# Optimization experiments

Hardware: AMD Instinct MI355X
Metric: run time of the kernel (lower is better)

## Reference

```python
import jax, jax.numpy as jnp
import numpy as np

N_NODES = 50000
N_EDGES = 800000
D_IN = 128
D_OUT = 128


def setup_inputs() -> dict:
    key = jax.random.key(0)
    k1, k2, k3, k4, k5 = jax.random.split(key, 5)
    x = jax.random.normal(k1, (N_NODES, D_IN), dtype=jnp.float32)
    edge_index = jax.random.randint(k2, (2, N_EDGES), 0, N_NODES, dtype=jnp.int64)
    # PyG SAGEConv params: lin_l (neighbors, with bias), lin_r (root, no bias)
    scale = 1.0 / np.sqrt(D_IN)
    W_l = jax.random.uniform(k3, (D_OUT, D_IN), dtype=jnp.float32, minval=-scale, maxval=scale)
    b_l = jax.random.uniform(k4, (D_OUT,), dtype=jnp.float32, minval=-scale, maxval=scale)
    W_r = jax.random.uniform(k5, (D_OUT, D_IN), dtype=jnp.float32, minval=-scale, maxval=scale)
    return {"x": x, "edge_index": edge_index, "W_l": W_l, "b_l": b_l, "W_r": W_r}


def reference(x, edge_index, W_l, b_l, W_r):
    src, dst = edge_index[0], edge_index[1]
    # mean aggregation of neighbor (source) features into destination nodes
    msg = x[src]  # [E, D_IN]
    agg_sum = jax.ops.segment_sum(msg, dst, num_segments=N_NODES)  # [N, D_IN]
    deg = jax.ops.segment_sum(jnp.ones((N_EDGES,), dtype=x.dtype), dst, num_segments=N_NODES)
    agg = agg_sum / jnp.maximum(deg, 1.0)[:, None]  # isolated nodes -> 0
    # out = lin_l(agg) + lin_r(x); ReLU from SAGE_NET wrapper (active=True)
    out = agg @ W_l.T + b_l + x @ W_r.T
    return jax.nn.relu(out)
```

## Files before the change

kernel.cpp:

```cpp
#include <hip/hip_runtime.h>
#include <hip/hip_bf16.h>

#define NNODES 50000
#define NEDGES 800000
#define DD 128
#define NPART 8
#define PSIZE 6250
#define CAP 64
#define NGROUPS 3910
#define WK_B (NGROUPS * 8 + 64)
#define WP2 68
#define ZROW ((u32)NNODES)

typedef unsigned int u32;
typedef unsigned short u16;
typedef short bf16x8 __attribute__((ext_vector_type(8)));
typedef float f32x4 __attribute__((ext_vector_type(4)));
typedef float f32x2 __attribute__((ext_vector_type(2)));

#if defined(__has_builtin)
#if __has_builtin(__builtin_amdgcn_cvt_pk_f32_fp8)
#define HAVE_HW_FP8 1
#endif
#endif

union U4B8 {
    uint4 u;
    bf16x8 b;
};

__device__ __forceinline__ u32 f2b(float f) {
    u32 u = __float_as_uint(f);
    u32 rounding = 0x7fffu + ((u >> 16) & 1u);
    return (u + rounding) >> 16;
}

__device__ __forceinline__ u32 f2e4m3(float f) {
    u32 u = __float_as_uint(f);
    u32 s = (u >> 31) << 7;
    u32 mag = u & 0x7fffffffu;
    if (mag < 0x3c800000u) return s;
    u32 t = mag + 0x0007FFFFu + ((mag >> 20) & 1u);
    u32 e = (t >> 23) - 120u;
    u32 m = (t >> 20) & 7u;
    if (e > 15u || (e == 15u && m == 7u)) { e = 15u; m = 6u; }
    return s | (e << 3) | m;
}

__device__ __forceinline__ void fp8x4_acc(u32 v, float& a0, float& a1,
                                          float& a2, float& a3) {
#ifdef HAVE_HW_FP8
    f32x2 lo = __builtin_amdgcn_cvt_pk_f32_fp8((int)v, false);
    f32x2 hi = __builtin_amdgcn_cvt_pk_f32_fp8((int)v, true);
    a0 += lo.x;
    a1 += lo.y;
    a2 += hi.x;
    a3 += hi.y;
#else
#pragma unroll
    for (int b = 0; b < 4; ++b) {
        u32 byte = (v >> (8 * b)) & 0xffu;
        u32 f = ((byte >> 7) << 31) | ((((byte >> 3) & 15u) + 120u) << 23) |
                ((byte & 7u) << 20);
        float val = (byte & 0x78u) ? __uint_as_float(f) : 0.f;
        if (b == 0) a0 += val;
        else if (b == 1) a1 += val;
        else if (b == 2) a2 += val;
        else a3 += val;
    }
#endif
}

__global__ __launch_bounds__(256) void work_k(
    const int* __restrict__ ei, u32* __restrict__ deg,
    u16* __restrict__ slots16, const float* __restrict__ x,
    u32* __restrict__ xb, u32* __restrict__ xq,
    const float* __restrict__ Wl, const float* __restrict__ Wr,
    u32* __restrict__ wb) {
    const int b = blockIdx.x, tid = threadIdx.x;
    if (b < NGROUPS * 8) {
        const u32 g = (u32)b >> 3, r8 = (u32)b & 7u;
        const u32 gm = g % 5u, gq = g / 5u;
        if (gm < 4u) {
            u32 fg = gq * 4u + gm;
            if (fg < 3125u) {
                u32 e = fg * 256u + tid;
                int dst = ei[NEDGES + e];
                if ((u32)(dst - r8 * PSIZE) < (u32)PSIZE) {
                    u32 pos = atomicAdd(deg + dst, 1u);
                    if (pos < CAP) slots16[(size_t)dst * CAP + pos] = (u16)ei[e];
                }
            }
        } else {
            u32 xi = gq * 8u + r8;
            if (xi < 6250u) {
                int i = (int)xi * 256 + tid;
                float4 v = ((const float4*)x)[i];
                uint2 o;
                o.x = f2b(v.x) | (f2b(v.y) << 16);
                o.y = f2b(v.z) | (f2b(v.w) << 16);
                ((uint2*)xb)[i] = o;
                xq[i] = f2e4m3(v.x) | (f2e4m3(v.y) << 8) | (f2e4m3(v.z) << 16) |
                        (f2e4m3(v.w) << 24);
            }
        }
    } else {
        int idx = (b - NGROUPS * 8) * 256 + tid;
        int o = idx >> 7, c = idx & 127, k0 = 2 * c;
        const float* src = (k0 < DD) ? (Wl + o * DD + k0) : (Wr + o * DD + (k0 - DD));
        wb[idx] = f2b(src[0]) | (f2b(src[1]) << 16);
        if (b == WK_B - 1 && tid < 32)
            xq[(size_t)ZROW * 32 + tid] = 0u;
    }
}

__global__ __launch_bounds__(512, 4) void sage_fused_k(
    const u32* __restrict__ xq, const u16* __restrict__ slots16,
    const u32* __restrict__ deg, const u32* __restrict__ xb,
    const u32* __restrict__ wb, const float* __restrict__ bl,
    float* __restrict__ out) {
    __shared__ u32 w2[DD * WP2];
    __shared__ u32 agg_lds[64 * WP2];
    __shared__ float sbias[DD];
    const int tid = threadIdx.x;
    const int row0 = blockIdx.x * 64;
    const int wave = tid >> 6, lane = tid & 63;
    const int m = lane & 15, quad = lane >> 4;
    const int rw = wave & 3;
    const int ch = wave >> 2;

    for (int r = tid >> 5; r < DD; r += 16) {
        int c2 = (tid & 31) * 2;
        *(uint2*)&w2[r * WP2 + c2] = *(const uint2*)&wb[r * DD + c2];
    }
    if (tid < DD) sbias[tid] = bl[tid];

    uint4 af_x[4];
    {
        int r = row0 + rw * 16 + m;
        r = r < NNODES ? r : NNODES - 1;
        const u32* xrow = xb + (size_t)r * 64;
#pragma unroll
        for (int ks = 0; ks < 4; ++ks)
            af_x[ks] = *(const uint4*)&xrow[ks * 16 + quad * 4];
    }

    const u32 half = lane >> 5;
    const u32 q = lane & 31u;
    const u32 nbase = (u32)(row0 + wave * 8);

    u32 dv[8], svv[8];
#pragma unroll
    for (int i = 0; i < 8; ++i) {
        u32 nn = nbase + (u32)i;
        bool ok = nn < (u32)NNODES;
        dv[i] = ok ? deg[nn] : 0u;
        svv[i] = ok ? (u32)slots16[(size_t)nn * CAP + lane] : 0u;
    }

#pragma unroll
    for (int i = 0; i < 8; ++i) {
        u32 d = dv[i];
        u32 cnt = min(d, (u32)CAP);
        u32 svp = (lane < cnt) ? svv[i] : ZROW;
        float a0 = 0.f, a1 = 0.f, a2 = 0.f, a3 = 0.f;
        for (u32 j = 0; j < cnt; j += 16) {
            u32 v[8];
#pragma unroll
            for (int p = 0; p < 8; ++p) {
                u32 sA = __shfl(svp, (int)(j + 2 * p), 64);
                u32 sB = __shfl(svp, (int)(j + 2 * p + 1), 64);
                u32 s = half ? sB : sA;
                v[p] = xq[(size_t)s * 32 + q];
            }
#pragma unroll
            for (int p = 0; p < 8; ++p) fp8x4_acc(v[p], a0, a1, a2, a3);
        }
        a0 += __shfl_xor(a0, 32, 64);
        a1 += __shfl_xor(a1, 32, 64);
        a2 += __shfl_xor(a2, 32, 64);
        a3 += __shfl_xor(a3, 32, 64);
        if (lane < 32) {
            float inv = 1.0f / fmaxf((float)d, 1.0f);
            uint2 o;
            o.x = f2b(a0 * inv) | (f2b(a1 * inv) << 16);
            o.y = f2b(a2 * inv) | (f2b(a3 * inv) << 16);
            *(uint2*)&agg_lds[(wave * 8 + i) * WP2 + q * 2] = o;
        }
    }
    __syncthreads();

    f32x4 acc[4];
#pragma unroll
    for (int nt = 0; nt < 4; ++nt) acc[nt] = (f32x4){0.f, 0.f, 0.f, 0.f};

#pragma unroll
    for (int ks = 0; ks < 4; ++ks) {
        U4B8 af;
        af.u = *(const uint4*)&agg_lds[(rw * 16 + m) * WP2 + ks * 16 + quad * 4];
#pragma unroll
        for (int nt = 0; nt < 4; ++nt) {
            U4B8 bf;
            bf.u = *(const uint4*)&w2[((ch * 4 + nt) * 16 + m) * WP2 + ks * 16 +
                                      quad * 4];
            acc[nt] = __builtin_amdgcn_mfma_f32_16x16x32_bf16(af.b, bf.b,
                                                              acc[nt], 0, 0, 0);
        }
    }
    __syncthreads();
    for (int r = tid >> 5; r < DD; r += 16) {
        int c2 = (tid & 31) * 2;
        *(uint2*)&w2[r * WP2 + c2] = *(const uint2*)&wb[r * DD + 64 + c2];
    }
    __syncthreads();

#pragma unroll
    for (int ks = 0; ks < 4; ++ks) {
        U4B8 af;
        af.u = af_x[ks];
#pragma unroll
        for (int nt = 0; nt < 4; ++nt) {
            U4B8 bf;
            bf.u = *(const uint4*)&w2[((ch * 4 + nt) * 16 + m) * WP2 + ks * 16 +
                                      quad * 4];
            acc[nt] = __builtin_amdgcn_mfma_f32_16x16x32_bf16(af.b, bf.b,
                                                              acc[nt], 0, 0, 0);
        }
    }

#pragma unroll
    for (int nt = 0; nt < 4; ++nt) {
        int col = (ch * 4 + nt) * 16 + m;
        float b = sbias[col];
#pragma unroll
        for (int r_ = 0; r_ < 4; ++r_) {
            int row = row0 + rw * 16 + quad * 4 + r_;
            if (row < NNODES)
                out[(size_t)row * DD + col] = fmaxf(acc[nt][r_] + b, 0.f);
        }
    }
}

__global__ __launch_bounds__(256) void scatter_k(
    const float* __restrict__ x, const int* __restrict__ ei,
    float* __restrict__ agg, u32* __restrict__ deg) {
    u32 gid = blockIdx.x * 256u + threadIdx.x;
    u32 edge = gid >> 6;
    u32 lane = gid & 63u;
    if (edge >= NEDGES) return;
    int src = ei[edge];
    int dst = ei[NEDGES + edge];
    float2 v = ((const float2*)(x + (size_t)src * DD))[lane];
    float* p = agg + (size_t)dst * DD + lane * 2u;
    unsafeAtomicAdd(p, v.x);
    unsafeAtomicAdd(p + 1, v.y);
    if (lane == 0) atomicAdd(deg + dst, 1u);
}

__global__ __launch_bounds__(256) void mean_k(
    float* __restrict__ agg, const u32* __restrict__ deg) {
    u32 gid = blockIdx.x * 256u + threadIdx.x;
    u32 node = gid >> 6;
    u32 lane = gid & 63u;
    if (node >= NNODES) return;
    float inv = 1.0f / fmaxf((float)deg[node], 1.0f);
    float2* p = (float2*)(agg + (size_t)node * DD) + lane;
    float2 v = *p;
    *p = make_float2(v.x * inv, v.y * inv);
}

__global__ __launch_bounds__(256) void lin_l_k(
    float* __restrict__ agg,
    const float* __restrict__ Wl, const float* __restrict__ bl) {
    __shared__ u32 WT[DD * 65];
    __shared__ float rows[4 * DD];
    __shared__ float sbias[DD];
    const int tid = threadIdx.x;
    {
        u16* WTs = (u16*)WT;
        for (int i = tid; i < DD * DD; i += 256) {
            int o = i >> 7, k = i & 127;
            WTs[k * 130 + o] = (u16)f2b(Wl[i]);
        }
        if (tid < DD) sbias[tid] = bl[tid];
    }
    __syncthreads();
    const int h = tid & 63;
    const int nl = tid >> 6;
    for (int base = blockIdx.x * 4; base < NNODES; base += gridDim.x * 4) {
        ((float2*)rows)[tid] =
            ((const float2*)(agg + (size_t)(base + (tid >> 6)) * DD))[tid & 63];
        __syncthreads();
        float acc0 = sbias[2 * h], acc1 = sbias[2 * h + 1];
#pragma unroll
        for (int k = 0; k < DD; ++k) {
            float a = rows[nl * DD + k];
            u32 w2 = WT[k * 65 + h];
            acc0 = fmaf(a, __uint_as_float(w2 << 16), acc0);
            acc1 = fmaf(a, __uint_as_float(w2 & 0xffff0000u), acc1);
        }
        __syncthreads();
        ((float2*)(agg + (size_t)(base + nl) * DD))[h] = make_float2(acc0, acc1);
    }
}

__global__ __launch_bounds__(256) void lin_r_k(
    float* __restrict__ io, const float* __restrict__ x,
    const float* __restrict__ Wr) {
    __shared__ u32 WT[DD * 65];
    __shared__ float rows[4 * DD];
    const int tid = threadIdx.x;
    {
        u16* WTs = (u16*)WT;
        for (int i = tid; i < DD * DD; i += 256) {
            int o = i >> 7, k = i & 127;
            WTs[k * 130 + o] = (u16)f2b(Wr[i]);
        }
    }
    __syncthreads();
    const int h = tid & 63;
    const int nl = tid >> 6;
    for (int base = blockIdx.x * 4; base < NNODES; base += gridDim.x * 4) {
        ((float2*)rows)[tid] =
            ((const float2*)(x + (size_t)(base + (tid >> 6)) * DD))[tid & 63];
        __syncthreads();
        float2 t2 = ((const float2*)(io + (size_t)(base + nl) * DD))[h];
        float acc0 = t2.x, acc1 = t2.y;
#pragma unroll
        for (int k = 0; k < DD; ++k) {
            float a = rows[nl * DD + k];
            u32 w2 = WT[k * 65 + h];
            acc0 = fmaf(a, __uint_as_float(w2 << 16), acc0);
            acc1 = fmaf(a, __uint_as_float(w2 & 0xffff0000u), acc1);
        }
        acc0 = fmaxf(acc0, 0.f);
        acc1 = fmaxf(acc1, 0.f);
        __syncthreads();
        ((float2*)(io + (size_t)(base + nl) * DD))[h] = make_float2(acc0, acc1);
    }
}

extern "C" void kernel_launch(void* const* d_in, const int* in_sizes, int n_in,
                              void* d_out, int out_size, void* d_ws, size_t ws_size,
                              hipStream_t stream) {
    const float* x  = (const float*)d_in[0];
    const int*   ei = (const int*)d_in[1];
    const float* Wl = (const float*)d_in[2];
    const float* bl = (const float*)d_in[3];
    const float* Wr = (const float*)d_in[4];

    u32* deg     = (u32*)d_ws;
    u16* slots16 = (u16*)(deg + NNODES);
    u32* wb      = (u32*)d_ws + NNODES + (size_t)NNODES * (CAP / 2);
    u32* xb      = wb + 16384;
    u32* xq      = xb + (size_t)NNODES * 64;
    const size_t need =
        ((size_t)NNODES * (1 + CAP / 2 + 64 + 32) + 16384 + 32) * 4;

    if (ws_size >= need) {
        hipMemsetAsync(deg, 0, (size_t)NNODES * sizeof(u32), stream);
        work_k<<<WK_B, 256, 0, stream>>>(
            ei, deg, slots16, x, xb, xq, Wl, Wr, wb);
        sage_fused_k<<<(NNODES + 63) / 64, 512, 0, stream>>>(
            xq, slots16, deg, xb, wb, bl, (float*)d_out);
    } else {
        float* agg = (float*)d_out;
        hipMemsetAsync(d_out, 0, (size_t)NNODES * DD * sizeof(float), stream);
        hipMemsetAsync(d_ws, 0, (size_t)NNODES * sizeof(u32), stream);
        scatter_k<<<(NEDGES * 64) / 256, 256, 0, stream>>>(x, ei, agg, deg);
        mean_k<<<(NNODES * 64 + 255) / 256, 256, 0, stream>>>(agg, deg);
        lin_l_k<<<1024, 256, 0, stream>>>(agg, Wl, bl);
        lin_r_k<<<1024, 256, 0, stream>>>(agg, x, Wr);
    }
}
```

Baseline: 163.7 us.

## Software-pipeline neighbor gathers across batches and nodes in aggregation loop

Restructures the per-wave mean-aggregation loop into a flat software pipeline: the next batch of 16 fp8 neighbor-row loads is issued (including the first batch of the next node) before the current batch is accumulated, hiding gather latency across node boundaries. The up-front loading of all 8 nodes' degree and slot lists is replaced by a one-node-ahead prefetch, and the x-row fragment loads for the MFMA are moved after the aggregation phase. This doubles the gather register buffers and adds loop-control branching, which may raise VGPR pressure and reduce occupancy.

```diff
diff --git a/kernel.cpp b/kernel.cpp
--- a/kernel.cpp
+++ b/kernel.cpp
@@ -69,6 +69,17 @@
         else a3 += val;
     }
 #endif
+}
+
+__device__ __forceinline__ void issue8(const u32* __restrict__ xq, u32 svp,
+                                       u32 j, u32 half, u32 q, u32 v[8]) {
+#pragma unroll
+    for (int p = 0; p < 8; ++p) {
+        u32 sA = __shfl(svp, (int)(j + 2u * p), 64);
+        u32 sB = __shfl(svp, (int)(j + 2u * p + 1u), 64);
+        u32 s = half ? sB : sA;
+        v[p] = xq[(size_t)s * 32 + q];
+    }
 }
 
 __global__ __launch_bounds__(256) void work_k(
@@ -135,6 +146,80 @@
     }
     if (tid < DD) sbias[tid] = bl[tid];
 
+    const u32 half = lane >> 5;
+    const u32 q = lane & 31u;
+    const u32 nbase = (u32)(row0 + wave * 8);
+
+    u32 d_cur = 0, sv_cur = 0;
+    if (nbase < (u32)NNODES) {
+        d_cur = deg[nbase];
+        sv_cur = (u32)slots16[(size_t)nbase * CAP + lane];
+    }
+    u32 d_nxt = 0, sv_nxt = 0;
+    if (nbase + 1u < (u32)NNODES) {
+        d_nxt = deg[nbase + 1u];
+        sv_nxt = (u32)slots16[(size_t)(nbase + 1u) * CAP + lane];
+    }
+
+    u32 cnt = min(d_cur, (u32)CAP);
+    u32 nb = cnt ? ((cnt + 15u) >> 4) : 1u;
+    u32 svp = (lane < cnt) ? sv_cur : ZROW;
+    u32 ddiv = d_cur;
+
+    float a0 = 0.f, a1 = 0.f, a2 = 0.f, a3 = 0.f;
+    u32 vb[8], vn[8];
+    issue8(xq, svp, 0u, half, q, vb);
+
+    int i = 0;
+    u32 b = 0;
+    u32 cnt_n = 0, nb_n = 0, svp_n = 0, ddiv_n = 0;
+    for (;;) {
+        const bool last_b = (b + 1u >= nb);
+        const bool have_next = !(last_b && i == 7);
+        if (have_next) {
+            if (!last_b) {
+                issue8(xq, svp, (b + 1u) * 16u, half, q, vn);
+            } else {
+                cnt_n = min(d_nxt, (u32)CAP);
+                nb_n = cnt_n ? ((cnt_n + 15u) >> 4) : 1u;
+                svp_n = (lane < cnt_n) ? sv_nxt : ZROW;
+                ddiv_n = d_nxt;
+                issue8(xq, svp_n, 0u, half, q, vn);
+            }
+        }
+#pragma unroll
+        for (int p = 0; p < 8; ++p) fp8x4_acc(vb[p], a0, a1, a2, a3);
+        if (last_b) {
+            a0 += __shfl_xor(a0, 32, 64);
+            a1 += __shfl_xor(a1, 32, 64);
+            a2 += __shfl_xor(a2, 32, 64);
+            a3 += __shfl_xor(a3, 32, 64);
+            if (lane < 32) {
+                float inv = 1.0f / fmaxf((float)ddiv, 1.0f);
+                uint2 o;
+                o.x = f2b(a0 * inv) | (f2b(a1 * inv) << 16);
+                o.y = f2b(a2 * inv) | (f2b(a3 * inv) << 16);
+                *(uint2*)&agg_lds[(wave * 8 + i) * WP2 + q * 2] = o;
+            }
+            a0 = a1 = a2 = a3 = 0.f;
+            ++i;
+            if (i == 8) break;
+            cnt = cnt_n; nb = nb_n; svp = svp_n; ddiv = ddiv_n;
+            b = 0;
+            u32 nn = nbase + (u32)i + 1u;
+            d_nxt = 0; sv_nxt = 0;
+            if (i < 7 && nn < (u32)NNODES) {
+                d_nxt = deg[nn];
+                sv_nxt = (u32)slots16[(size_t)nn * CAP + lane];
+            }
+        } else {
+            ++b;
+        }
+#pragma unroll
+        for (int p = 0; p < 8; ++p) vb[p] = vn[p];
+    }
+    __syncthreads();
+
     uint4 af_x[4];
     {
         int r = row0 + rw * 16 + m;
@@ -144,51 +229,6 @@
         for (int ks = 0; ks < 4; ++ks)
             af_x[ks] = *(const uint4*)&xrow[ks * 16 + quad * 4];
     }
-
-    const u32 half = lane >> 5;
-    const u32 q = lane & 31u;
-    const u32 nbase = (u32)(row0 + wave * 8);
-
-    u32 dv[8], svv[8];
-#pragma unroll
-    for (int i = 0; i < 8; ++i) {
-        u32 nn = nbase + (u32)i;
-        bool ok = nn < (u32)NNODES;
-        dv[i] = ok ? deg[nn] : 0u;
-        svv[i] = ok ? (u32)slots16[(size_t)nn * CAP + lane] : 0u;
-    }
-
-#pragma unroll
-    for (int i = 0; i < 8; ++i) {
-        u32 d = dv[i];
-        u32 cnt = min(d, (u32)CAP);
-        u32 svp = (lane < cnt) ? svv[i] : ZROW;
-        float a0 = 0.f, a1 = 0.f, a2 = 0.f, a3 = 0.f;
-        for (u32 j = 0; j < cnt; j += 16) {
-            u32 v[8];
-#pragma unroll
-            for (int p = 0; p < 8; ++p) {
-                u32 sA = __shfl(svp, (int)(j + 2 * p), 64);
-                u32 sB = __shfl(svp, (int)(j + 2 * p + 1), 64);
-                u32 s = half ? sB : sA;
-                v[p] = xq[(size_t)s * 32 + q];
-            }
-#pragma unroll
-            for (int p = 0; p < 8; ++p) fp8x4_acc(v[p], a0, a1, a2, a3);
-        }
-        a0 += __shfl_xor(a0, 32, 64);
-        a1 += __shfl_xor(a1, 32, 64);
-        a2 += __shfl_xor(a2, 32, 64);
-        a3 += __shfl_xor(a3, 32, 64);
-        if (lane < 32) {
-            float inv = 1.0f / fmaxf((float)d, 1.0f);
-            uint2 o;
-            o.x = f2b(a0 * inv) | (f2b(a1 * inv) << 16);
-            o.y = f2b(a2 * inv) | (f2b(a3 * inv) << 16);
-            *(uint2*)&agg_lds[(wave * 8 + i) * WP2 + q * 2] = o;
-        }
-    }
-    __syncthreads();
 
     f32x4 acc[4];
 #pragma unroll
```

Measured after the change: 166.1 us. About the same (+1.5%).

## Split fused gather+GEMM kernel into separate gather and GEMM kernels

Applied to the files above, without the earlier changes.

Splits the fused kernel in two. A standalone gather kernel runs one wave per node and writes the bf16 mean aggregates to a workspace buffer. A separate GEMM kernel then loads those aggregates from global memory straight into MFMA operand registers. The aim is to decouple the latency-bound random gather from the LDS-heavy GEMM, so the gather can run at higher occupancy without the GEMM's shared-memory footprint. The cost is an extra kernel launch and an extra round trip of the aggregate buffer (about 12.8 MB) through global memory.

```diff
diff --git a/kernel.cpp b/kernel.cpp
--- a/kernel.cpp
+++ b/kernel.cpp
@@ -114,13 +114,49 @@
     }
 }
 
-__global__ __launch_bounds__(512, 4) void sage_fused_k(
+__global__ __launch_bounds__(256) void gather_k(
     const u32* __restrict__ xq, const u16* __restrict__ slots16,
-    const u32* __restrict__ deg, const u32* __restrict__ xb,
+    const u32* __restrict__ deg, u32* __restrict__ aggb) {
+    u32 gid = blockIdx.x * 256u + threadIdx.x;
+    u32 node = gid >> 6;
+    u32 lane = gid & 63u;
+    if (node >= NNODES) return;
+    u32 d = deg[node];
+    u32 cnt = min(d, (u32)CAP);
+    u32 svp = (lane < cnt) ? (u32)slots16[(size_t)node * CAP + lane] : ZROW;
+    const u32 half = lane >> 5;
+    const u32 q = lane & 31u;
+    float a0 = 0.f, a1 = 0.f, a2 = 0.f, a3 = 0.f;
+    for (u32 j = 0; j < cnt; j += 16) {
+        u32 v[8];
+#pragma unroll
+        for (int p = 0; p < 8; ++p) {
+            u32 sA = __shfl(svp, (int)(j + 2 * p), 64);
+            u32 sB = __shfl(svp, (int)(j + 2 * p + 1), 64);
+            u32 s = half ? sB : sA;
+            v[p] = xq[(size_t)s * 32 + q];
+        }
+#pragma unroll
+        for (int p = 0; p < 8; ++p) fp8x4_acc(v[p], a0, a1, a2, a3);
+    }
+    a0 += __shfl_xor(a0, 32, 64);
+    a1 += __shfl_xor(a1, 32, 64);
+    a2 += __shfl_xor(a2, 32, 64);
+    a3 += __shfl_xor(a3, 32, 64);
+    if (lane < 32) {
+        float inv = 1.0f / fmaxf((float)d, 1.0f);
+        uint2 o;
+        o.x = f2b(a0 * inv) | (f2b(a1 * inv) << 16);
+        o.y = f2b(a2 * inv) | (f2b(a3 * inv) << 16);
+        *(uint2*)&aggb[(size_t)node * 64 + q * 2] = o;
+    }
+}
+
+__global__ __launch_bounds__(512, 4) void gemm_k(
+    const u32* __restrict__ aggb, const u32* __restrict__ xb,
     const u32* __restrict__ wb, const float* __restrict__ bl,
     float* __restrict__ out) {
     __shared__ u32 w2[DD * WP2];
-    __shared__ u32 agg_lds[64 * WP2];
     __shared__ float sbias[DD];
     const int tid = threadIdx.x;
     const int row0 = blockIdx.x * 64;
@@ -129,65 +165,24 @@
     const int rw = wave & 3;
     const int ch = wave >> 2;
 
+    uint4 af_a[4], af_x[4];
+    {
+        int r = row0 + rw * 16 + m;
+        r = r < NNODES ? r : NNODES - 1;
+        const u32* arow = aggb + (size_t)r * 64;
+        const u32* xrow = xb + (size_t)r * 64;
+#pragma unroll
+        for (int ks = 0; ks < 4; ++ks) {
+            af_a[ks] = *(const uint4*)&arow[ks * 16 + quad * 4];
+            af_x[ks] = *(const uint4*)&xrow[ks * 16 + quad * 4];
+        }
+    }
+
     for (int r = tid >> 5; r < DD; r += 16) {
         int c2 = (tid & 31) * 2;
         *(uint2*)&w2[r * WP2 + c2] = *(const uint2*)&wb[r * DD + c2];
     }
     if (tid < DD) sbias[tid] = bl[tid];
-
-    uint4 af_x[4];
-    {
-        int r = row0 + rw * 16 + m;
-        r = r < NNODES ? r : NNODES - 1;
-        const u32* xrow = xb + (size_t)r * 64;
-#pragma unroll
-        for (int ks = 0; ks < 4; ++ks)
-            af_x[ks] = *(const uint4*)&xrow[ks * 16 + quad * 4];
-    }
-
-    const u32 half = lane >> 5;
-    const u32 q = lane & 31u;
-    const u32 nbase = (u32)(row0 + wave * 8);
-
-    u32 dv[8], svv[8];
-#pragma unroll
-    for (int i = 0; i < 8; ++i) {
-        u32 nn = nbase + (u32)i;
-        bool ok = nn < (u32)NNODES;
-        dv[i] = ok ? deg[nn] : 0u;
-        svv[i] = ok ? (u32)slots16[(size_t)nn * CAP + lane] : 0u;
-    }
-
-#pragma unroll
-    for (int i = 0; i < 8; ++i) {
-        u32 d = dv[i];
-        u32 cnt = min(d, (u32)CAP);
-        u32 svp = (lane < cnt) ? svv[i] : ZROW;
-        float a0 = 0.f, a1 = 0.f, a2 = 0.f, a3 = 0.f;
-        for (u32 j = 0; j < cnt; j += 16) {
-            u32 v[8];
-#pragma unroll
-            for (int p = 0; p < 8; ++p) {
-                u32 sA = __shfl(svp, (int)(j + 2 * p), 64);
-                u32 sB = __shfl(svp, (int)(j + 2 * p + 1), 64);
-                u32 s = half ? sB : sA;
-                v[p] = xq[(size_t)s * 32 + q];
-            }
-#pragma unroll
-            for (int p = 0; p < 8; ++p) fp8x4_acc(v[p], a0, a1, a2, a3);
-        }
-        a0 += __shfl_xor(a0, 32, 64);
-        a1 += __shfl_xor(a1, 32, 64);
-        a2 += __shfl_xor(a2, 32, 64);
-        a3 += __shfl_xor(a3, 32, 64);
-        if (lane < 32) {
-            float inv = 1.0f / fmaxf((float)d, 1.0f);
-            uint2 o;
-            o.x = f2b(a0 * inv) | (f2b(a1 * inv) << 16);
-            o.y = f2b(a2 * inv) | (f2b(a3 * inv) << 16);
-            *(uint2*)&agg_lds[(wave * 8 + i) * WP2 + q * 2] = o;
-        }
-    }
     __syncthreads();
 
     f32x4 acc[4];
@@ -197,7 +192,7 @@
 #pragma unroll
     for (int ks = 0; ks < 4; ++ks) {
         U4B8 af;
-        af.u = *(const uint4*)&agg_lds[(rw * 16 + m) * WP2 + ks * 16 + quad * 4];
+        af.u = af_a[ks];
 #pragma unroll
         for (int nt = 0; nt < 4; ++nt) {
             U4B8 bf;
@@ -354,15 +349,17 @@
     u32* wb      = (u32*)d_ws + NNODES + (size_t)NNODES * (CAP / 2);
     u32* xb      = wb + 16384;
     u32* xq      = xb + (size_t)NNODES * 64;
+    u32* aggb    = xq + (size_t)NNODES * 32 + 32;
     const size_t need =
-        ((size_t)NNODES * (1 + CAP / 2 + 64 + 32) + 16384 + 32) * 4;
+        ((size_t)NNODES * (1 + CAP / 2 + 64 + 32 + 64) + 16384 + 32) * 4;
 
     if (ws_size >= need) {
         hipMemsetAsync(deg, 0, (size_t)NNODES * sizeof(u32), stream);
         work_k<<<WK_B, 256, 0, stream>>>(
             ei, deg, slots16, x, xb, xq, Wl, Wr, wb);
-        sage_fused_k<<<(NNODES + 63) / 64, 512, 0, stream>>>(
-            xq, slots16, deg, xb, wb, bl, (float*)d_out);
+        gather_k<<<12500, 256, 0, stream>>>(xq, slots16, deg, aggb);
+        gemm_k<<<(NNODES + 63) / 64, 512, 0, stream>>>(
+            aggb, xb, wb, bl, (float*)d_out);
     } else {
         float* agg = (float*)d_out;
         hipMemsetAsync(d_out, 0, (size_t)NNODES * DD * sizeof(float), stream);
```

New measurement: 156.8 us. 4.2% less time.
